# Kernel optimization log

Measured on AMD Instinct MI355X. Metric: run time of the kernel, lower is better.

Reference implementation:

```python
import jax, jax.numpy as jnp
import numpy as np

N, E, C, D, M = 20000, 640000, 128, 128, 128


def setup_inputs() -> dict:
    key = jax.random.key(0)
    ks = jax.random.split(key, 16)
    g = lambda k, shape, fan: jax.random.normal(k, shape, jnp.float32) * (1.0 / np.sqrt(fan))
    return {
        "x": jax.random.normal(ks[0], (N, C), jnp.float32),
        "edge_index": jax.random.randint(ks[1], (2, E), 0, N, jnp.int64),
        "W_src": g(ks[2], (C, D), C),
        "b_src": jnp.zeros((D,), jnp.float32),
        "W_tgt": g(ks[3], (C, D), C),
        "W_skip": g(ks[4], (C, D), C),
        "a0": jnp.asarray(0.2, jnp.float32),   # PReLU init=0.2
        "W1": g(ks[5], (D, M), D),
        "b1": jnp.zeros((M,), jnp.float32),
        "a1": jnp.asarray(0.25, jnp.float32),  # MLP PReLU default
        "W2": g(ks[6], (M, D), M),
        "b2": jnp.zeros((D,), jnp.float32),
        "Wg": g(ks[7], (D, 1), D),
        "gamma": jnp.ones((D,), jnp.float32),
        "beta": jnp.zeros((D,), jnp.float32),
    }


def _prelu(h, a):
    return jnp.where(h >= 0, h, a * h)


def reference(x, edge_index, W_src, b_src, W_tgt, W_skip, a0, W1, b1, a1, W2, b2, Wg, gamma, beta):
    n = x.shape[0]
    j, i = edge_index[0], edge_index[1]  # src -> tgt
    msg_src = x @ W_src + b_src          # lin_src (bias)
    msg_tgt = x @ W_tgt                  # lin_tgt (no bias)
    # per-edge message: msg_nn(msg_j + msg_i) = PReLU -> Linear -> PReLU -> Linear
    h = _prelu(msg_src[j] + msg_tgt[i], a0)          # [E, D]
    h = _prelu(h @ W1 + b1, a1)                      # [E, M]
    msg = h @ W2 + b2                                # [E, D]
    # gate + sparse softmax over edges grouped by target node i
    gate = msg @ Wg                                  # [E, 1]
    gmax = jax.ops.segment_max(gate, i, num_segments=n)
    eg = jnp.exp(gate - gmax[i])
    gsum = jax.ops.segment_sum(eg, i, num_segments=n)
    alpha = eg / (gsum[i] + 1e-16)                   # [E, 1]
    # aggregate (aggr='add')
    out = jax.ops.segment_sum(alpha * msg, i, num_segments=n)  # [N, D]
    # root/skip connection
    out = out + x @ W_skip
    # LayerNorm
    mu = jnp.mean(out, axis=-1, keepdims=True)
    var = jnp.var(out, axis=-1, keepdims=True)
    out = (out - mu) * jax.lax.rsqrt(var + 1e-5) * gamma + beta
    return out
```

## Files before the change

### kernel.cpp

```cpp
#include <hip/hip_runtime.h>
#include <hip/hip_bf16.h>
#include <stdint.h>

#define DIM 128
#define HSTR 136
#define NMAX 20224

using hfrag = __attribute__((ext_vector_type(8))) _Float16;
using h2v   = __attribute__((ext_vector_type(2))) _Float16;
using f32x4 = __attribute__((ext_vector_type(4))) float;
using f32x2 = __attribute__((ext_vector_type(2))) float;

__device__ __forceinline__ float prelu_f(float v, float a) { return v >= 0.f ? v : a * v; }

__device__ __forceinline__ unsigned pkh(float a, float b) {
    auto h = __builtin_amdgcn_cvt_pkrtz(a, b);
    return *(unsigned*)&h;
}
__device__ __forceinline__ unsigned prelu2_add(unsigned su, unsigned gu, h2v a2) {
    h2v s = *(h2v*)&su, g = *(h2v*)&gu;
    h2v h = s + g;
    h2v z = {(_Float16)0.f, (_Float16)0.f};
    h2v mx = __builtin_elementwise_max(h, z);
    h2v mn = __builtin_elementwise_min(h, z);
    h2v r = mn * a2 + mx;
    return *(unsigned*)&r;
}

__global__ __launch_bounds__(256) void prep_hist_k(
    const float* __restrict__ Wsrc, const float* __restrict__ Wtgt,
    const float* __restrict__ Wskip, const float* __restrict__ W1,
    const float* __restrict__ W2, const float* __restrict__ b2,
    const float* __restrict__ Wg,
    unsigned short* __restrict__ Wall, float* __restrict__ w2g,
    const int* __restrict__ eidx, int E, int* __restrict__ deg,
    int* __restrict__ rank)
{
    const int nhist = (E + 255) / 256;
    if ((int)blockIdx.x < nhist) {
        const int e = blockIdx.x * 256 + threadIdx.x;
        if (e < E) rank[e] = atomicAdd(deg + eidx[(size_t)E + e], 1);
        return;
    }
    const int b = blockIdx.x - nhist;
    if (b == (5 * DIM * DIM) / 256) {
        const int k = threadIdx.x;
        if (k < DIM) {
            float s = 0.f;
            for (int d = 0; d < DIM; ++d) s += W2[k * DIM + d] * Wg[d];
            w2g[k] = s;
        } else if (k == DIM) {
            float s = 0.f;
            for (int d = 0; d < DIM; ++d) s += b2[d] * Wg[d];
            w2g[DIM] = s;
        }
        return;
    }
    const int idx = b * 256 + threadIdx.x;
    const int m = idx >> 14;
    const int r = idx & 16383;
    const int n = r >> 7, k = r & 127;
    const float* W = (m == 0) ? Wsrc : (m == 1) ? Wtgt : (m == 2) ? Wskip : (m == 3) ? W1 : W2;
    const _Float16 hv = (_Float16)W[k * DIM + n];
    Wall[idx] = *(const unsigned short*)&hv;
}

__global__ __launch_bounds__(256) void scan_k(const int* __restrict__ deg,
                                              int* __restrict__ rowptr, int N)
{
    __shared__ int part[256];
    const int t = threadIdx.x;

    if (N <= NMAX) {
        __shared__ int s[NMAX];
        for (int k = t; k < N; k += 256) s[k] = deg[k];
        __syncthreads();

        const int chunk = (N + 255) / 256;
        const int lo = min(t * chunk, N), hi = min(lo + chunk, N);
        int sum = 0;
        for (int k = lo; k < hi; ++k) sum += s[k];
        part[t] = sum;
        __syncthreads();
        for (int off = 1; off < 256; off <<= 1) {
            int u = (t >= off) ? part[t - off] : 0;
            __syncthreads();
            part[t] += u;
            __syncthreads();
        }
        int run = part[t] - sum;
        for (int k = lo; k < hi; ++k) { const int d = s[k]; s[k] = run; run += d; }
        __syncthreads();
        for (int k = t; k < N; k += 256) rowptr[k] = s[k];
        if (t == 0) rowptr[N] = part[255];
    } else {
        const int chunk = (N + 255) / 256;
        const int lo = min(t * chunk, N), hi = min(lo + chunk, N);
        int s = 0;
        for (int k = lo; k < hi; ++k) s += deg[k];
        part[t] = s;
        __syncthreads();
        for (int off = 1; off < 256; off <<= 1) {
            int u = (t >= off) ? part[t - off] : 0;
            __syncthreads();
            part[t] += u;
            __syncthreads();
        }
        int run = part[t] - s;
        for (int k = lo; k < hi; ++k) {
            rowptr[k] = run;
            run += deg[k];
        }
        if (t == 255) rowptr[N] = part[255];
    }
}

__global__ __launch_bounds__(256) void scatter_node_k(
    const int* __restrict__ eidx, int E,
    const int* __restrict__ rowptr, const int* __restrict__ rank,
    int2* __restrict__ jip, int nscatter,
    const float* __restrict__ x,
    const unsigned short* __restrict__ Wall,
    const float* __restrict__ bsrc,
    unsigned short* __restrict__ msg_src, unsigned short* __restrict__ msg_tgt,
    float* __restrict__ skip, int N)
{
    if ((int)blockIdx.x < nscatter) {
        const int e = blockIdx.x * 256 + threadIdx.x;
        if (e < E) {
            const int j = eidx[e];
            const int i = eidx[(size_t)E + e];
            const int p = rowptr[i] + rank[e];
            jip[p] = make_int2(j, i);
        }
        return;
    }

    __shared__ unsigned short xt[32 * HSTR];
    const int t = threadIdx.x;
    const int n0blk = (blockIdx.x - nscatter) * 32;
    const int w = t >> 6, lane = t & 63, col = lane & 15, quad = lane >> 4;

    for (int k = t; k < 32 * 16; k += 256) {
        const int row = k >> 4, o = k & 15;
        uint4 v = make_uint4(0, 0, 0, 0);
        if (n0blk + row < N) {
            const float4 a = *(const float4*)(x + (size_t)(n0blk + row) * DIM + o * 8);
            const float4 b = *(const float4*)(x + (size_t)(n0blk + row) * DIM + o * 8 + 4);
            v.x = pkh(a.x, a.y); v.y = pkh(a.z, a.w);
            v.z = pkh(b.x, b.y); v.w = pkh(b.z, b.w);
        }
        *(uint4*)(xt + row * HSTR + o * 8) = v;
    }
    __syncthreads();

    hfrag af[2][4];
    #pragma unroll
    for (int mt = 0; mt < 2; ++mt)
        #pragma unroll
        for (int ks = 0; ks < 4; ++ks)
            af[mt][ks] = *(const hfrag*)(xt + (mt * 16 + col) * HSTR + ks * 32 + quad * 8);

    for (int m = 0; m < 3; ++m) {
        const unsigned short* Wt = Wall + m * DIM * DIM;
        hfrag bw[2][4];
        #pragma unroll
        for (int nt = 0; nt < 2; ++nt)
            #pragma unroll
            for (int ks = 0; ks < 4; ++ks)
                bw[nt][ks] = *(const hfrag*)(Wt + (w * 32 + nt * 16 + col) * DIM + ks * 32 + quad * 8);

        f32x4 acc[2][2];
        #pragma unroll
        for (int mt = 0; mt < 2; ++mt)
            #pragma unroll
            for (int nt = 0; nt < 2; ++nt)
                acc[mt][nt] = f32x4{0.f, 0.f, 0.f, 0.f};

        #pragma unroll
        for (int mt = 0; mt < 2; ++mt)
            #pragma unroll
            for (int nt = 0; nt < 2; ++nt)
                #pragma unroll
                for (int ks = 0; ks < 4; ++ks)
                    acc[mt][nt] = __builtin_amdgcn_mfma_f32_16x16x32_f16(
                        bw[nt][ks], af[mt][ks], acc[mt][nt], 0, 0, 0);

        #pragma unroll
        for (int mt = 0; mt < 2; ++mt) {
            const int node = n0blk + mt * 16 + col;
            if (node >= N) continue;
            #pragma unroll
            for (int nt = 0; nt < 2; ++nt) {
                const int f0 = w * 32 + nt * 16 + quad * 4;
                if (m == 2) {
                    float4 o;
                    o.x = acc[mt][nt][0]; o.y = acc[mt][nt][1];
                    o.z = acc[mt][nt][2]; o.w = acc[mt][nt][3];
                    *(float4*)(skip + (size_t)node * DIM + f0) = o;
                } else {
                    float b0 = 0.f, b1v = 0.f, b2v = 0.f, b3v = 0.f;
                    if (m == 0) {
                        const float4 bb = *(const float4*)(bsrc + f0);
                        b0 = bb.x; b1v = bb.y; b2v = bb.z; b3v = bb.w;
                    }
                    uint2 o;
                    o.x = pkh(acc[mt][nt][0] + b0, acc[mt][nt][1] + b1v);
                    o.y = pkh(acc[mt][nt][2] + b2v, acc[mt][nt][3] + b3v);
                    unsigned short* dst = (m == 0) ? msg_src : msg_tgt;
                    *(uint2*)(dst + (size_t)node * DIM + f0) = o;
                }
            }
        }
    }
}

__global__ __launch_bounds__(256, 3) void edge_mlp_mfma(
    const int2* __restrict__ jip, int ntiles,
    const unsigned short* __restrict__ msg_src, const unsigned short* __restrict__ msg_tgt,
    const float* __restrict__ a0p,
    const unsigned short* __restrict__ W1t, const float* __restrict__ b1,
    const float* __restrict__ a1p,
    const float* __restrict__ w2g,
    unsigned char* __restrict__ h2buf,
    float* __restrict__ gate)
{
    __shared__ unsigned short h1[2][64 * HSTR];
    __shared__ float gate_part[2][4][64];

    const int t = threadIdx.x;
    const float a0 = *a0p, a1 = *a1p;
    const h2v a02 = {(_Float16)a0, (_Float16)a0};
    const int w = t >> 6, lane = t & 63, col = lane & 15, quad = lane >> 4;
    const int o = t & 15, r0 = t >> 4;

    hfrag bw1[2][4];
    float4 b1q[2], wgq[2];
    #pragma unroll
    for (int nt = 0; nt < 2; ++nt) {
        const int n = w * 32 + nt * 16 + col;
        #pragma unroll
        for (int ks = 0; ks < 4; ++ks)
            bw1[nt][ks] = *(const hfrag*)(W1t + n * DIM + ks * 32 + quad * 8);
        const int nq = w * 32 + nt * 16 + quad * 4;
        b1q[nt] = *(const float4*)(b1 + nq);
        wgq[nt] = *(const float4*)(w2g + nq);
    }
    const float c2 = w2g[DIM];
    const int stride = gridDim.x;

    int tile = blockIdx.x;
    if (tile >= ntiles) return;

    int2 eA[4], eB[4];
    uint4 svA[4], svB[4], gvA[4], gvB[4];

    {
        const int p0 = tile * 64;
        #pragma unroll
        for (int i = 0; i < 4; ++i) eA[i] = jip[p0 + r0 + 16 * i];
        #pragma unroll
        for (int i = 0; i < 4; ++i) {
            svA[i] = *(const uint4*)(msg_src + (size_t)eA[i].x * DIM + o * 8);
            gvA[i] = *(const uint4*)(msg_tgt + (size_t)eA[i].y * DIM + o * 8);
        }
        const int tn = tile + stride;
        const int p1 = (tn < ntiles ? tn : tile) * 64;
        #pragma unroll
        for (int i = 0; i < 4; ++i) eB[i] = jip[p1 + r0 + 16 * i];
    }

    int buf = 0;
    int prev_p0 = -1;

    for (; tile < ntiles; tile += stride) {
        const int p0 = tile * 64;

        #pragma unroll
        for (int i = 0; i < 4; ++i) {
            svB[i] = *(const uint4*)(msg_src + (size_t)eB[i].x * DIM + o * 8);
            gvB[i] = *(const uint4*)(msg_tgt + (size_t)eB[i].y * DIM + o * 8);
        }

        #pragma unroll
        for (int i = 0; i < 4; ++i) {
            uint4 hv;
            hv.x = prelu2_add(svA[i].x, gvA[i].x, a02);
            hv.y = prelu2_add(svA[i].y, gvA[i].y, a02);
            hv.z = prelu2_add(svA[i].z, gvA[i].z, a02);
            hv.w = prelu2_add(svA[i].w, gvA[i].w, a02);
            *(uint4*)(h1[buf] + (r0 + 16 * i) * HSTR + o * 8) = hv;
        }

        #pragma unroll
        for (int i = 0; i < 4; ++i) eA[i] = eB[i];
        {
            const int tnn = tile + 2 * stride;
            const int p2 = (tnn < ntiles ? tnn : tile) * 64;
            #pragma unroll
            for (int i = 0; i < 4; ++i) eB[i] = jip[p2 + r0 + 16 * i];
        }

        __syncthreads();

        if (prev_p0 >= 0 && t < 64)
            gate[prev_p0 + t] = gate_part[1 - buf][0][t] + gate_part[1 - buf][1][t]
                              + gate_part[1 - buf][2][t] + gate_part[1 - buf][3][t] + c2;

        f32x4 acc[4][2];
        #pragma unroll
        for (int mt = 0; mt < 4; ++mt)
            #pragma unroll
            for (int nt = 0; nt < 2; ++nt)
                acc[mt][nt] = f32x4{0.f, 0.f, 0.f, 0.f};

        #pragma unroll
        for (int mt = 0; mt < 4; ++mt) {
            hfrag af[4];
            #pragma unroll
            for (int ks = 0; ks < 4; ++ks)
                af[ks] = *(const hfrag*)(h1[buf] + (mt * 16 + col) * HSTR + ks * 32 + quad * 8);
            #pragma unroll
            for (int nt = 0; nt < 2; ++nt)
                #pragma unroll
                for (int ks = 0; ks < 4; ++ks)
                    acc[mt][nt] = __builtin_amdgcn_mfma_f32_16x16x32_f16(
                        bw1[nt][ks], af[ks], acc[mt][nt], 0, 0, 0);
        }

        #pragma unroll
        for (int mt = 0; mt < 4; ++mt) {
            const int m = mt * 16 + col;
            float g = 0.f;
            #pragma unroll
            for (int nt = 0; nt < 2; ++nt) {
                const int n0 = w * 32 + nt * 16 + quad * 4;
                const float p0v = prelu_f(acc[mt][nt][0] + b1q[nt].x, a1);
                const float p1v = prelu_f(acc[mt][nt][1] + b1q[nt].y, a1);
                const float p2v = prelu_f(acc[mt][nt][2] + b1q[nt].z, a1);
                const float p3v = prelu_f(acc[mt][nt][3] + b1q[nt].w, a1);
                int pk = __builtin_amdgcn_cvt_pk_fp8_f32(p0v, p1v, 0, false);
                pk = __builtin_amdgcn_cvt_pk_fp8_f32(p2v, p3v, pk, true);
                *(unsigned*)(h2buf + (size_t)(p0 + m) * DIM + n0) = (unsigned)pk;
                g += p0v * wgq[nt].x + p1v * wgq[nt].y + p2v * wgq[nt].z + p3v * wgq[nt].w;
            }
            g += __shfl_xor(g, 16);
            g += __shfl_xor(g, 32);
            if (quad == 0) gate_part[buf][w][m] = g;
        }

        #pragma unroll
        for (int i = 0; i < 4; ++i) { svA[i] = svB[i]; gvA[i] = gvB[i]; }
        prev_p0 = p0;
        buf ^= 1;
    }

    __syncthreads();
    if (t < 64)
        gate[prev_p0 + t] = gate_part[1 - buf][0][t] + gate_part[1 - buf][1][t]
                          + gate_part[1 - buf][2][t] + gate_part[1 - buf][3][t] + c2;
}

__global__ __launch_bounds__(256) void aggregate_h2_k(
    const int* __restrict__ rowptr,
    const float* __restrict__ gate, const unsigned char* __restrict__ h2buf,
    unsigned short* __restrict__ aggh2, int N)
{
    const int n = blockIdx.x * 4 + (threadIdx.x >> 6);
    const int lane = threadIdx.x & 63;
    if (n >= N) return;

    const int base = rowptr[n];
    const int deg = rowptr[n + 1] - base;
    const int grp = lane >> 4, sub = lane & 15;

    float acc[8] = {0.f, 0.f, 0.f, 0.f, 0.f, 0.f, 0.f, 0.f};
    float se = 0.f;
    for (int k = grp; k < deg; k += 4) {
        const float e = __expf(fminf(gate[base + k], 60.f));
        se += e;
        const uint2 mv = *(const uint2*)(h2buf + (size_t)(base + k) * DIM + sub * 8);
        const f32x2 f01 = __builtin_amdgcn_cvt_pk_f32_fp8(mv.x, false);
        const f32x2 f23 = __builtin_amdgcn_cvt_pk_f32_fp8(mv.x, true);
        const f32x2 f45 = __builtin_amdgcn_cvt_pk_f32_fp8(mv.y, false);
        const f32x2 f67 = __builtin_amdgcn_cvt_pk_f32_fp8(mv.y, true);
        acc[0] += e * f01.x; acc[1] += e * f01.y;
        acc[2] += e * f23.x; acc[3] += e * f23.y;
        acc[4] += e * f45.x; acc[5] += e * f45.y;
        acc[6] += e * f67.x; acc[7] += e * f67.y;
    }
    #pragma unroll
    for (int j = 0; j < 8; ++j) {
        acc[j] += __shfl_xor(acc[j], 16);
        acc[j] += __shfl_xor(acc[j], 32);
    }
    se += __shfl_xor(se, 16);
    se += __shfl_xor(se, 32);
    const float inv = 1.f / (se + 1e-16f);

    if (grp == 0) {
        uint4 ov;
        ov.x = pkh(acc[0] * inv, acc[1] * inv);
        ov.y = pkh(acc[2] * inv, acc[3] * inv);
        ov.z = pkh(acc[4] * inv, acc[5] * inv);
        ov.w = pkh(acc[6] * inv, acc[7] * inv);
        *(uint4*)(aggh2 + (size_t)n * DIM + sub * 8) = ov;
    }
}

__global__ __launch_bounds__(256) void node_out_k(
    const unsigned short* __restrict__ aggh2,
    const unsigned short* __restrict__ W2t, const float* __restrict__ b2,
    const float* __restrict__ skip,
    const float* __restrict__ gamma, const float* __restrict__ beta,
    float* __restrict__ out, int N)
{
    __shared__ unsigned short hh[64 * HSTR];
    __shared__ float ls1[4][4][16], ls2[4][4][16];

    const int t = threadIdx.x;
    const int n0blk = blockIdx.x * 64;
    const int w = t >> 6, lane = t & 63, col = lane & 15, quad = lane >> 4;

    hfrag bw2[2][4];
    float4 b2q[2];
    #pragma unroll
    for (int nt = 0; nt < 2; ++nt) {
        const int n = w * 32 + nt * 16 + col;
        #pragma unroll
        for (int ks = 0; ks < 4; ++ks)
            bw2[nt][ks] = *(const hfrag*)(W2t + n * DIM + ks * 32 + quad * 8);
        b2q[nt] = *(const float4*)(b2 + w * 32 + nt * 16 + quad * 4);
    }

    for (int k = t; k < 64 * 16; k += 256) {
        const int row = k >> 4, o = k & 15;
        uint4 v = make_uint4(0, 0, 0, 0);
        if (n0blk + row < N) v = *(const uint4*)(aggh2 + (size_t)(n0blk + row) * DIM + o * 8);
        *(uint4*)(hh + row * HSTR + o * 8) = v;
    }
    __syncthreads();

    f32x4 acc[4][2];
    #pragma unroll
    for (int mt = 0; mt < 4; ++mt)
        #pragma unroll
        for (int nt = 0; nt < 2; ++nt)
            acc[mt][nt] = f32x4{0.f, 0.f, 0.f, 0.f};

    #pragma unroll
    for (int mt = 0; mt < 4; ++mt) {
        hfrag af[4];
        #pragma unroll
        for (int ks = 0; ks < 4; ++ks)
            af[ks] = *(const hfrag*)(hh + (mt * 16 + col) * HSTR + ks * 32 + quad * 8);
        #pragma unroll
        for (int nt = 0; nt < 2; ++nt)
            #pragma unroll
            for (int ks = 0; ks < 4; ++ks)
                acc[mt][nt] = __builtin_amdgcn_mfma_f32_16x16x32_f16(
                    bw2[nt][ks], af[ks], acc[mt][nt], 0, 0, 0);
    }

    float v[4][2][4];
    #pragma unroll
    for (int mt = 0; mt < 4; ++mt) {
        const int node = n0blk + mt * 16 + col;
        float s1 = 0.f, s2 = 0.f;
        #pragma unroll
        for (int nt = 0; nt < 2; ++nt) {
            const int f0 = w * 32 + nt * 16 + quad * 4;
            float4 sk = make_float4(0.f, 0.f, 0.f, 0.f);
            if (node < N) sk = *(const float4*)(skip + (size_t)node * DIM + f0);
            v[mt][nt][0] = acc[mt][nt][0] + b2q[nt].x + sk.x;
            v[mt][nt][1] = acc[mt][nt][1] + b2q[nt].y + sk.y;
            v[mt][nt][2] = acc[mt][nt][2] + b2q[nt].z + sk.z;
            v[mt][nt][3] = acc[mt][nt][3] + b2q[nt].w + sk.w;
            #pragma unroll
            for (int r = 0; r < 4; ++r) {
                s1 += v[mt][nt][r];
                s2 += v[mt][nt][r] * v[mt][nt][r];
            }
        }
        s1 += __shfl_xor(s1, 16); s1 += __shfl_xor(s1, 32);
        s2 += __shfl_xor(s2, 16); s2 += __shfl_xor(s2, 32);
        if (quad == 0) { ls1[w][mt][col] = s1; ls2[w][mt][col] = s2; }
    }
    __syncthreads();

    #pragma unroll
    for (int mt = 0; mt < 4; ++mt) {
        const int node = n0blk + mt * 16 + col;
        if (node >= N) continue;
        const float sum = ls1[0][mt][col] + ls1[1][mt][col] + ls1[2][mt][col] + ls1[3][mt][col];
        const float sq  = ls2[0][mt][col] + ls2[1][mt][col] + ls2[2][mt][col] + ls2[3][mt][col];
        const float mu = sum * (1.f / 128.f);
        const float var = sq * (1.f / 128.f) - mu * mu;
        const float rs = rsqrtf(var + 1e-5f);
        #pragma unroll
        for (int nt = 0; nt < 2; ++nt) {
            const int f0 = w * 32 + nt * 16 + quad * 4;
            const float4 gm = *(const float4*)(gamma + f0);
            const float4 bt = *(const float4*)(beta + f0);
            float4 ov;
            ov.x = (v[mt][nt][0] - mu) * rs * gm.x + bt.x;
            ov.y = (v[mt][nt][1] - mu) * rs * gm.y + bt.y;
            ov.z = (v[mt][nt][2] - mu) * rs * gm.z + bt.z;
            ov.w = (v[mt][nt][3] - mu) * rs * gm.w + bt.w;
            *(float4*)(out + (size_t)node * DIM + f0) = ov;
        }
    }
}

extern "C" void kernel_launch(void* const* d_in, const int* in_sizes, int n_in,
                              void* d_out, int out_size, void* d_ws, size_t ws_size,
                              hipStream_t stream)
{
    const float* x     = (const float*)d_in[0];
    const int*   eidx  = (const int*)d_in[1];
    const float* Wsrc  = (const float*)d_in[2];
    const float* bsrc  = (const float*)d_in[3];
    const float* Wtgt  = (const float*)d_in[4];
    const float* Wskip = (const float*)d_in[5];
    const float* a0    = (const float*)d_in[6];
    const float* W1    = (const float*)d_in[7];
    const float* b1    = (const float*)d_in[8];
    const float* a1    = (const float*)d_in[9];
    const float* W2    = (const float*)d_in[10];
    const float* b2    = (const float*)d_in[11];
    const float* Wg    = (const float*)d_in[12];
    const float* gamma = (const float*)d_in[13];
    const float* beta  = (const float*)d_in[14];

    const int N = in_sizes[0] / DIM;
    const int E = in_sizes[1] / 2;
    const int Npad = ((N + 63) / 64) * 64;
    float* out = (float*)d_out;

    char* ws = (char*)d_ws;
    size_t off = 0;
    auto alloc = [&](size_t bytes) -> void* {
        void* p = ws + off;
        off += (bytes + 255) & ~(size_t)255;
        return p;
    };
    unsigned short* msg_src = (unsigned short*)alloc((size_t)N * DIM * 2);
    unsigned short* msg_tgt = (unsigned short*)alloc((size_t)N * DIM * 2);
    float*          skip    = (float*)alloc((size_t)N * DIM * 4);
    float*          gate    = (float*)alloc((size_t)E * 4);
    int*            deg     = (int*)alloc((size_t)N * 4);
    int*            rowptr  = (int*)alloc((size_t)(N + 1) * 4);
    int*            rank    = (int*)alloc((size_t)E * 4);
    int2*           jip     = (int2*)alloc((size_t)E * 8);
    unsigned short* Wall    = (unsigned short*)alloc((size_t)5 * DIM * DIM * 2);
    float*          w2g     = (float*)alloc((size_t)(DIM + 1) * 4);
    unsigned short* aggh2   = (unsigned short*)alloc((size_t)Npad * DIM * 2);
    unsigned char*  h2buf   = (unsigned char*)alloc((size_t)E * DIM);
    (void)ws_size; (void)n_in; (void)out_size;

    (void)hipMemsetAsync(deg, 0, (size_t)N * 4, stream);

    const int nhist = (E + 255) / 256;
    prep_hist_k<<<nhist + (5 * DIM * DIM) / 256 + 1, 256, 0, stream>>>(
        Wsrc, Wtgt, Wskip, W1, W2, b2, Wg, Wall, w2g, eidx, E, deg, rank);

    scan_k<<<1, 256, 0, stream>>>(deg, rowptr, N);

    const int nscatter = (E + 255) / 256;
    const int nnode = (N + 31) / 32;
    scatter_node_k<<<nscatter + nnode, 256, 0, stream>>>(
        eidx, E, rowptr, rank, jip, nscatter,
        x, Wall, bsrc, msg_src, msg_tgt, skip, N);

    const int ntiles = E / 64;
    const int egrid = ntiles < 1024 ? ntiles : 1024;
    edge_mlp_mfma<<<egrid, 256, 0, stream>>>(jip, ntiles, msg_src, msg_tgt, a0,
                                             Wall + 3 * DIM * DIM, b1, a1,
                                             w2g, h2buf, gate);

    aggregate_h2_k<<<(N + 3) / 4, 256, 0, stream>>>(rowptr, gate, h2buf, aggh2, N);

    node_out_k<<<Npad / 64, 256, 0, stream>>>(aggh2, Wall + 4 * DIM * DIM, b2, skip,
                                              gamma, beta, out, N);
}
```

Baseline: 256.3 us.

## Fuse edge softmax-weighted aggregation into edge MLP kernel via MFMA and atomics

The edge MLP kernel no longer writes per-edge FP8 hidden activations and gates to global memory. It now computes exp(gate) in-kernel and forms a segment-indicator matrix over the target nodes spanned by each sorted 64-edge tile. It multiplies that matrix with the transposed hidden tile in LDS using MFMA and atomically adds the partial sums S and normaliser Z into global memory. The separate aggregate kernel is removed and node_out now normalises S by Z. This removes the large E×128 intermediate round-trip and a launch. In exchange it adds float atomics, an extra barrier per tile, and loses the max-subtraction, relying on a fixed clamp at 11 instead.

```diff
diff --git a/kernel.cpp b/kernel.cpp
--- a/kernel.cpp
+++ b/kernel.cpp
@@ -4,6 +4,7 @@
 
 #define DIM 128
 #define HSTR 136
+#define H2STR 72
 #define NMAX 20224
 
 using hfrag = __attribute__((ext_vector_type(8))) _Float16;
@@ -16,6 +17,10 @@
 __device__ __forceinline__ unsigned pkh(float a, float b) {
     auto h = __builtin_amdgcn_cvt_pkrtz(a, b);
     return *(unsigned*)&h;
+}
+__device__ __forceinline__ unsigned short hs(float v) {
+    _Float16 h = (_Float16)v;
+    return *(unsigned short*)&h;
 }
 __device__ __forceinline__ unsigned prelu2_add(unsigned su, unsigned gu, h2v a2) {
     h2v s = *(h2v*)&su, g = *(h2v*)&gu;
@@ -215,18 +220,19 @@
     }
 }
 
-__global__ __launch_bounds__(256, 3) void edge_mlp_mfma(
+__global__ __launch_bounds__(256, 4) void edge_mlp_fused(
     const int2* __restrict__ jip, int ntiles,
     const unsigned short* __restrict__ msg_src, const unsigned short* __restrict__ msg_tgt,
     const float* __restrict__ a0p,
     const unsigned short* __restrict__ W1t, const float* __restrict__ b1,
     const float* __restrict__ a1p,
     const float* __restrict__ w2g,
-    unsigned char* __restrict__ h2buf,
-    float* __restrict__ gate)
+    float* __restrict__ S, float* __restrict__ Z)
 {
-    __shared__ unsigned short h1[2][64 * HSTR];
-    __shared__ float gate_part[2][4][64];
+    __shared__ unsigned short h1[64 * HSTR];
+    __shared__ unsigned short h2t[DIM * H2STR];
+    __shared__ float gate_part[4][64];
+    __shared__ int il_lds[2][64];
 
     const int t = threadIdx.x;
     const float a0 = *a0p, a1 = *a1p;
@@ -270,12 +276,9 @@
         for (int i = 0; i < 4; ++i) eB[i] = jip[p1 + r0 + 16 * i];
     }
 
-    int buf = 0;
-    int prev_p0 = -1;
+    int par = 0;
 
     for (; tile < ntiles; tile += stride) {
-        const int p0 = tile * 64;
-
         #pragma unroll
         for (int i = 0; i < 4; ++i) {
             svB[i] = *(const uint4*)(msg_src + (size_t)eB[i].x * DIM + o * 8);
@@ -289,7 +292,8 @@
             hv.y = prelu2_add(svA[i].y, gvA[i].y, a02);
             hv.z = prelu2_add(svA[i].z, gvA[i].z, a02);
             hv.w = prelu2_add(svA[i].w, gvA[i].w, a02);
-            *(uint4*)(h1[buf] + (r0 + 16 * i) * HSTR + o * 8) = hv;
+            *(uint4*)(h1 + (r0 + 16 * i) * HSTR + o * 8) = hv;
+            if (o == 0) il_lds[par][r0 + 16 * i] = eA[i].y;
         }
 
         #pragma unroll
@@ -303,10 +307,6 @@
 
         __syncthreads();
 
-        if (prev_p0 >= 0 && t < 64)
-            gate[prev_p0 + t] = gate_part[1 - buf][0][t] + gate_part[1 - buf][1][t]
-                              + gate_part[1 - buf][2][t] + gate_part[1 - buf][3][t] + c2;
-
         f32x4 acc[4][2];
         #pragma unroll
         for (int mt = 0; mt < 4; ++mt)
@@ -319,7 +319,7 @@
             hfrag af[4];
             #pragma unroll
             for (int ks = 0; ks < 4; ++ks)
-                af[ks] = *(const hfrag*)(h1[buf] + (mt * 16 + col) * HSTR + ks * 32 + quad * 8);
+                af[ks] = *(const hfrag*)(h1 + (mt * 16 + col) * HSTR + ks * 32 + quad * 8);
             #pragma unroll
             for (int nt = 0; nt < 2; ++nt)
                 #pragma unroll
@@ -334,82 +334,100 @@
             float g = 0.f;
             #pragma unroll
             for (int nt = 0; nt < 2; ++nt) {
-                const int n0 = w * 32 + nt * 16 + quad * 4;
+                const int fb = w * 32 + nt * 16 + quad * 4;
                 const float p0v = prelu_f(acc[mt][nt][0] + b1q[nt].x, a1);
                 const float p1v = prelu_f(acc[mt][nt][1] + b1q[nt].y, a1);
                 const float p2v = prelu_f(acc[mt][nt][2] + b1q[nt].z, a1);
                 const float p3v = prelu_f(acc[mt][nt][3] + b1q[nt].w, a1);
-                int pk = __builtin_amdgcn_cvt_pk_fp8_f32(p0v, p1v, 0, false);
-                pk = __builtin_amdgcn_cvt_pk_fp8_f32(p2v, p3v, pk, true);
-                *(unsigned*)(h2buf + (size_t)(p0 + m) * DIM + n0) = (unsigned)pk;
+                h2t[(fb + 0) * H2STR + m] = hs(p0v);
+                h2t[(fb + 1) * H2STR + m] = hs(p1v);
+                h2t[(fb + 2) * H2STR + m] = hs(p2v);
+                h2t[(fb + 3) * H2STR + m] = hs(p3v);
                 g += p0v * wgq[nt].x + p1v * wgq[nt].y + p2v * wgq[nt].z + p3v * wgq[nt].w;
             }
             g += __shfl_xor(g, 16);
             g += __shfl_xor(g, 32);
-            if (quad == 0) gate_part[buf][w][m] = g;
+            if (quad == 0) gate_part[w][m] = g;
+        }
+
+        __syncthreads();
+
+        {
+            const int i0v = il_lds[par][0];
+            const int span = il_lds[par][63] - i0v;
+            for (int nl0 = 0; nl0 <= span; nl0 += 16) {
+                const int nbase = i0v + nl0;
+                const int rem = span - nl0;
+                hfrag bf2[2];
+                float zp = 0.f;
+                #pragma unroll
+                for (int ks = 0; ks < 2; ++ks) {
+                    const int e0 = ks * 32 + quad * 8;
+                    const float4 ga0 = *(const float4*)&gate_part[0][e0];
+                    const float4 ga1 = *(const float4*)&gate_part[1][e0];
+                    const float4 ga2 = *(const float4*)&gate_part[2][e0];
+                    const float4 ga3 = *(const float4*)&gate_part[3][e0];
+                    const float4 gb0 = *(const float4*)&gate_part[0][e0 + 4];
+                    const float4 gb1 = *(const float4*)&gate_part[1][e0 + 4];
+                    const float4 gb2 = *(const float4*)&gate_part[2][e0 + 4];
+                    const float4 gb3 = *(const float4*)&gate_part[3][e0 + 4];
+                    const int4 ia = *(const int4*)&il_lds[par][e0];
+                    const int4 ib = *(const int4*)&il_lds[par][e0 + 4];
+                    const float e0v = __expf(fminf(ga0.x + ga1.x + ga2.x + ga3.x + c2, 11.f));
+                    const float e1v = __expf(fminf(ga0.y + ga1.y + ga2.y + ga3.y + c2, 11.f));
+                    const float e2v = __expf(fminf(ga0.z + ga1.z + ga2.z + ga3.z + c2, 11.f));
+                    const float e3v = __expf(fminf(ga0.w + ga1.w + ga2.w + ga3.w + c2, 11.f));
+                    const float e4v = __expf(fminf(gb0.x + gb1.x + gb2.x + gb3.x + c2, 11.f));
+                    const float e5v = __expf(fminf(gb0.y + gb1.y + gb2.y + gb3.y + c2, 11.f));
+                    const float e6v = __expf(fminf(gb0.z + gb1.z + gb2.z + gb3.z + c2, 11.f));
+                    const float e7v = __expf(fminf(gb0.w + gb1.w + gb2.w + gb3.w + c2, 11.f));
+                    const float s0 = (ia.x - nbase == col) ? e0v : 0.f;
+                    const float s1 = (ia.y - nbase == col) ? e1v : 0.f;
+                    const float s2 = (ia.z - nbase == col) ? e2v : 0.f;
+                    const float s3 = (ia.w - nbase == col) ? e3v : 0.f;
+                    const float s4 = (ib.x - nbase == col) ? e4v : 0.f;
+                    const float s5 = (ib.y - nbase == col) ? e5v : 0.f;
+                    const float s6 = (ib.z - nbase == col) ? e6v : 0.f;
+                    const float s7 = (ib.w - nbase == col) ? e7v : 0.f;
+                    zp += s0 + s1 + s2 + s3 + s4 + s5 + s6 + s7;
+                    uint4 uu;
+                    uu.x = pkh(s0, s1); uu.y = pkh(s2, s3);
+                    uu.z = pkh(s4, s5); uu.w = pkh(s6, s7);
+                    bf2[ks] = *(hfrag*)&uu;
+                }
+                float z = zp;
+                z += __shfl_xor(z, 16);
+                z += __shfl_xor(z, 32);
+                if (w == 0 && quad == 0 && col <= rem)
+                    atomicAdd(Z + nbase + col, z);
+                #pragma unroll
+                for (int nt = 0; nt < 2; ++nt) {
+                    f32x4 r2 = f32x4{0.f, 0.f, 0.f, 0.f};
+                    #pragma unroll
+                    for (int ks = 0; ks < 2; ++ks) {
+                        const hfrag a2 = *(const hfrag*)(
+                            h2t + (w * 32 + nt * 16 + col) * H2STR + ks * 32 + quad * 8);
+                        r2 = __builtin_amdgcn_mfma_f32_16x16x32_f16(a2, bf2[ks], r2, 0, 0, 0);
+                    }
+                    if (col <= rem) {
+                        float* dst = S + (size_t)(nbase + col) * DIM + w * 32 + nt * 16 + quad * 4;
+                        atomicAdd(dst + 0, r2[0]);
+                        atomicAdd(dst + 1, r2[1]);
+                        atomicAdd(dst + 2, r2[2]);
+                        atomicAdd(dst + 3, r2[3]);
+                    }
+                }
+            }
         }
 
         #pragma unroll
         for (int i = 0; i < 4; ++i) { svA[i] = svB[i]; gvA[i] = gvB[i]; }
-        prev_p0 = p0;
-        buf ^= 1;
-    }
-
-    __syncthreads();
-    if (t < 64)
-        gate[prev_p0 + t] = gate_part[1 - buf][0][t] + gate_part[1 - buf][1][t]
-                          + gate_part[1 - buf][2][t] + gate_part[1 - buf][3][t] + c2;
-}
-
-__global__ __launch_bounds__(256) void aggregate_h2_k(
-    const int* __restrict__ rowptr,
-    const float* __restrict__ gate, const unsigned char* __restrict__ h2buf,
-    unsigned short* __restrict__ aggh2, int N)
-{
-    const int n = blockIdx.x * 4 + (threadIdx.x >> 6);
-    const int lane = threadIdx.x & 63;
-    if (n >= N) return;
-
-    const int base = rowptr[n];
-    const int deg = rowptr[n + 1] - base;
-    const int grp = lane >> 4, sub = lane & 15;
-
-    float acc[8] = {0.f, 0.f, 0.f, 0.f, 0.f, 0.f, 0.f, 0.f};
-    float se = 0.f;
-    for (int k = grp; k < deg; k += 4) {
-        const float e = __expf(fminf(gate[base + k], 60.f));
-        se += e;
-        const uint2 mv = *(const uint2*)(h2buf + (size_t)(base + k) * DIM + sub * 8);
-        const f32x2 f01 = __builtin_amdgcn_cvt_pk_f32_fp8(mv.x, false);
-        const f32x2 f23 = __builtin_amdgcn_cvt_pk_f32_fp8(mv.x, true);
-        const f32x2 f45 = __builtin_amdgcn_cvt_pk_f32_fp8(mv.y, false);
-        const f32x2 f67 = __builtin_amdgcn_cvt_pk_f32_fp8(mv.y, true);
-        acc[0] += e * f01.x; acc[1] += e * f01.y;
-        acc[2] += e * f23.x; acc[3] += e * f23.y;
-        acc[4] += e * f45.x; acc[5] += e * f45.y;
-        acc[6] += e * f67.x; acc[7] += e * f67.y;
-    }
-    #pragma unroll
-    for (int j = 0; j < 8; ++j) {
-        acc[j] += __shfl_xor(acc[j], 16);
-        acc[j] += __shfl_xor(acc[j], 32);
-    }
-    se += __shfl_xor(se, 16);
-    se += __shfl_xor(se, 32);
-    const float inv = 1.f / (se + 1e-16f);
-
-    if (grp == 0) {
-        uint4 ov;
-        ov.x = pkh(acc[0] * inv, acc[1] * inv);
-        ov.y = pkh(acc[2] * inv, acc[3] * inv);
-        ov.z = pkh(acc[4] * inv, acc[5] * inv);
-        ov.w = pkh(acc[6] * inv, acc[7] * inv);
-        *(uint4*)(aggh2 + (size_t)n * DIM + sub * 8) = ov;
+        par ^= 1;
     }
 }
 
 __global__ __launch_bounds__(256) void node_out_k(
-    const unsigned short* __restrict__ aggh2,
+    const float* __restrict__ S, const float* __restrict__ Z,
     const unsigned short* __restrict__ W2t, const float* __restrict__ b2,
     const float* __restrict__ skip,
     const float* __restrict__ gamma, const float* __restrict__ beta,
@@ -434,10 +452,19 @@
     }
 
     for (int k = t; k < 64 * 16; k += 256) {
-        const int row = k >> 4, o = k & 15;
+        const int row = k >> 4, oo = k & 15;
+        const int node = n0blk + row;
         uint4 v = make_uint4(0, 0, 0, 0);
-        if (n0blk + row < N) v = *(const uint4*)(aggh2 + (size_t)(n0blk + row) * DIM + o * 8);
-        *(uint4*)(hh + row * HSTR + o * 8) = v;
+        if (node < N) {
+            const float invz = 1.f / (Z[node] + 1e-16f);
+            const float4 a = *(const float4*)(S + (size_t)node * DIM + oo * 8);
+            const float4 b = *(const float4*)(S + (size_t)node * DIM + oo * 8 + 4);
+            v.x = pkh(a.x * invz, a.y * invz);
+            v.y = pkh(a.z * invz, a.w * invz);
+            v.z = pkh(b.x * invz, b.y * invz);
+            v.w = pkh(b.z * invz, b.w * invz);
+        }
+        *(uint4*)(hh + row * HSTR + oo * 8) = v;
     }
     __syncthreads();
 
@@ -544,21 +571,21 @@
         off += (bytes + 255) & ~(size_t)255;
         return p;
     };
+    float*          S       = (float*)alloc((size_t)N * DIM * 4);
+    float*          Zb      = (float*)alloc((size_t)N * 4);
+    int*            deg     = (int*)alloc((size_t)N * 4);
     unsigned short* msg_src = (unsigned short*)alloc((size_t)N * DIM * 2);
     unsigned short* msg_tgt = (unsigned short*)alloc((size_t)N * DIM * 2);
     float*          skip    = (float*)alloc((size_t)N * DIM * 4);
-    float*          gate    = (float*)alloc((size_t)E * 4);
-    int*            deg     = (int*)alloc((size_t)N * 4);
     int*            rowptr  = (int*)alloc((size_t)(N + 1) * 4);
     int*            rank    = (int*)alloc((size_t)E * 4);
     int2*           jip     = (int2*)alloc((size_t)E * 8);
     unsigned short* Wall    = (unsigned short*)alloc((size_t)5 * DIM * DIM * 2);
     float*          w2g     = (float*)alloc((size_t)(DIM + 1) * 4);
-    unsigned short* aggh2   = (unsigned short*)alloc((size_t)Npad * DIM * 2);
-    unsigned char*  h2buf   = (unsigned char*)alloc((size_t)E * DIM);
     (void)ws_size; (void)n_in; (void)out_size;
 
-    (void)hipMemsetAsync(deg, 0, (size_t)N * 4, stream);
+    const size_t zspan = (size_t)((char*)deg - (char*)S) + (size_t)N * 4;
+    (void)hipMemsetAsync(S, 0, zspan, stream);
 
     const int nhist = (E + 255) / 256;
     prep_hist_k<<<nhist + (5 * DIM * DIM) / 256 + 1, 256, 0, stream>>>(
@@ -574,12 +601,10 @@
 
     const int ntiles = E / 64;
     const int egrid = ntiles < 1024 ? ntiles : 1024;
-    edge_mlp_mfma<<<egrid, 256, 0, stream>>>(jip, ntiles, msg_src, msg_tgt, a0,
-                                             Wall + 3 * DIM * DIM, b1, a1,
-                                             w2g, h2buf, gate);
-
-    aggregate_h2_k<<<(N + 3) / 4, 256, 0, stream>>>(rowptr, gate, h2buf, aggh2, N);
-
-    node_out_k<<<Npad / 64, 256, 0, stream>>>(aggh2, Wall + 4 * DIM * DIM, b2, skip,
+    edge_mlp_fused<<<egrid, 256, 0, stream>>>(jip, ntiles, msg_src, msg_tgt, a0,
+                                              Wall + 3 * DIM * DIM, b1, a1,
+                                              w2g, S, Zb);
+
+    node_out_k<<<Npad / 64, 256, 0, stream>>>(S, Zb, Wall + 4 * DIM * DIM, b2, skip,
                                               gamma, beta, out, N);
 }
```

Result: slower. 371.4 us (+44.9%).
